# Performance work log

Hardware: AMD Instinct MI355X
Metric: run time of the kernel (lower is better)

## Reference

```python
import jax, jax.numpy as jnp
import numpy as np

N_ITER = 12
LR_PRIMAL = 0.5
LR_DUAL = 0.8
LAM_CLIP = 1e6
SLACK_EPS = 1e-8


def setup_inputs() -> dict:
    key = jax.random.key(0)
    k1, k2, k3 = jax.random.split(key, 3)
    B, n_gen = 65536, 256
    p_pred = jax.random.normal(k1, (B, n_gen), dtype=jnp.float32)
    p_min = jnp.zeros((n_gen,), dtype=jnp.float32)
    # generator upper limits in (1, 11)
    p_max = 1.0 + 10.0 * jax.random.uniform(k2, (n_gen,), dtype=jnp.float32)
    # total load roughly feasible: fraction of total capacity
    total_load = jax.random.uniform(k3, (B,), dtype=jnp.float32) * jnp.sum(p_max) * 0.5
    return {"p_pred": p_pred, "total_load": total_load, "p_min": p_min, "p_max": p_max}


def _dc_feasibility(p_pred, total_load, p_min, p_max):
    # p_pred: (B, n_gen); total_load: (B,)
    load = total_load[:, None]            # (B, 1)
    pmin = p_min[None, :]                 # (1, n_gen)
    pmax = p_max[None, :]
    p = p_pred
    lam = jnp.zeros((p.shape[0], 1), dtype=p.dtype)
    for _ in range(N_ITER):  # fixed unrolled primal-dual iterations
        grad = (p - p_pred) + lam
        p = p - LR_PRIMAL * grad
        p = jnp.clip(p, pmin, pmax)
        res = jnp.sum(p, axis=1, keepdims=True) - load
        lam = jnp.clip(lam + LR_DUAL * res, -LAM_CLIP, LAM_CLIP)
    # final slack redistribution among strictly-interior generators
    res = jnp.sum(p, axis=1, keepdims=True) - load
    slack_mask = ((p > pmin + SLACK_EPS) & (p < pmax - SLACK_EPS)).astype(p.dtype)
    slack_sum = jnp.sum(slack_mask, axis=1, keepdims=True)
    slack_sum = jnp.where(slack_sum == 0, jnp.ones_like(slack_sum), slack_sum)
    p = p - (res / slack_sum) * slack_mask
    return p


def reference(p_pred, total_load, p_min, p_max):
    return _dc_feasibility(p_pred, total_load, p_min, p_max)
```

## Files before the change

### kernel.cpp

```cpp
#include <hip/hip_runtime.h>

#define NITER 12

typedef float v2f __attribute__((ext_vector_type(2)));

__device__ __forceinline__ float dpp_ror_add(float x, const int ctrl_base) {
    int xi = __builtin_bit_cast(int, x);
    int yi;
    switch (ctrl_base) {
      case 8: yi = __builtin_amdgcn_update_dpp(0, xi, 0x128, 0xf, 0xf, true); break;
      case 4: yi = __builtin_amdgcn_update_dpp(0, xi, 0x124, 0xf, 0xf, true); break;
      case 2: yi = __builtin_amdgcn_update_dpp(0, xi, 0x122, 0xf, 0xf, true); break;
      default: yi = __builtin_amdgcn_update_dpp(0, xi, 0x121, 0xf, 0xf, true); break;
    }
    return x + __builtin_bit_cast(float, yi);
}

__global__ __launch_bounds__(256, 8) void dc_feas_kernel(
    const float* __restrict__ p_pred,
    const float* __restrict__ total_load,
    const float* __restrict__ p_min,
    const float* __restrict__ p_max,
    float* __restrict__ out, int B)
{
#pragma clang fp contract(off)
    const int lane = threadIdx.x & 63;
    const int wave = threadIdx.x >> 6;
    const int r    = lane >> 5;
    const int t    = lane & 31;

    const int row = (blockIdx.x << 3) + (wave << 1) + r;
    if (row >= B) return;

    const size_t base = (size_t)row * 256;
    const int e0 = t << 2;

    const float4 a0 = *(const float4*)(p_pred + base + e0);
    const float4 a1 = *(const float4*)(p_pred + base + e0 + 128);
    const float4 h0 = *(const float4*)(p_max + e0);
    const float4 h1 = *(const float4*)(p_max + e0 + 128);

    v2f PR[4], HI[4], P[4];
    PR[0] = (v2f){a0.x, a1.x}; PR[1] = (v2f){a0.y, a1.y};
    PR[2] = (v2f){a0.z, a1.z}; PR[3] = (v2f){a0.w, a1.w};
    HI[0] = (v2f){h0.x, h1.x}; HI[1] = (v2f){h0.y, h1.y};
    HI[2] = (v2f){h0.z, h1.z}; HI[3] = (v2f){h0.w, h1.w};

    const float load = total_load[row];

    auto rowsum = [&](const v2f* v) -> float {
        const v2f A = (v[0] + v[1]) + (v[2] + v[3]);
        float s = A.x + A.y;
        s += __shfl_xor(s, 16, 64);
        s = dpp_ror_add(s, 8);
        s = dpp_ror_add(s, 4);
        s = dpp_ror_add(s, 2);
        s = dpp_ror_add(s, 1);
        return s;
    };

#pragma unroll
    for (int j = 0; j < 4; ++j) {
        P[j].x = __builtin_amdgcn_fmed3f(PR[j].x, 0.0f, HI[j].x);
        P[j].y = __builtin_amdgcn_fmed3f(PR[j].y, 0.0f, HI[j].y);
    }
    float res = rowsum(P) - load;
    float lam = __builtin_amdgcn_fmed3f(0.8f * res, -1000000.0f, 1000000.0f);

    for (int it = 1; it < NITER; ++it) {
        const v2f lam2  = (v2f){lam, lam};
        const v2f mhalf = (v2f){-0.5f, -0.5f};
#pragma unroll
        for (int j = 0; j < 4; ++j) {
            const v2f g  = (P[j] - PR[j]) + lam2;
            const v2f pn = __builtin_elementwise_fma(g, mhalf, P[j]);
            P[j].x = __builtin_amdgcn_fmed3f(pn.x, 0.0f, HI[j].x);
            P[j].y = __builtin_amdgcn_fmed3f(pn.y, 0.0f, HI[j].y);
        }
        res = rowsum(P) - load;
        const float dl = 0.8f * res;
        lam = __builtin_amdgcn_fmed3f(lam + dl, -1000000.0f, 1000000.0f);
    }

    v2f M[4];
#pragma unroll
    for (int j = 0; j < 4; ++j) {
        M[j].x = (P[j].x > 1e-8f && P[j].x < HI[j].x - 1e-8f) ? 1.0f : 0.0f;
        M[j].y = (P[j].y > 1e-8f && P[j].y < HI[j].y - 1e-8f) ? 1.0f : 0.0f;
    }
    float ss = rowsum(M);
    ss = (ss == 0.0f) ? 1.0f : ss;
    const float adj = res / ss;

    const v2f madj2 = (v2f){-adj, -adj};
    v2f O[4];
#pragma unroll
    for (int j = 0; j < 4; ++j)
        O[j] = __builtin_elementwise_fma(M[j], madj2, P[j]);

    float4 o;
    o.x = O[0].x; o.y = O[1].x; o.z = O[2].x; o.w = O[3].x;
    *(float4*)(out + base + e0) = o;
    o.x = O[0].y; o.y = O[1].y; o.z = O[2].y; o.w = O[3].y;
    *(float4*)(out + base + e0 + 128) = o;
}

extern "C" void kernel_launch(void* const* d_in, const int* in_sizes, int n_in,
                              void* d_out, int out_size, void* d_ws, size_t ws_size,
                              hipStream_t stream) {
    const float* p_pred     = (const float*)d_in[0];
    const float* total_load = (const float*)d_in[1];
    const float* p_min      = (const float*)d_in[2];
    const float* p_max      = (const float*)d_in[3];
    float* out = (float*)d_out;

    const int B = in_sizes[1];
    const int rows_per_block = 8;
    const int grid = (B + rows_per_block - 1) / rows_per_block;

    dc_feas_kernel<<<grid, 256, 0, stream>>>(p_pred, total_load, p_min, p_max, out, B);
}
```

Before: 121.2 us.

## Use persistent grid-stride waves with software-prefetched next row pair

Replaces the one-row-pair-per-wave launch with a fixed grid of 2048 blocks in which each wave loops over row pairs with a grid stride. The next pair's p_pred and load values are loaded before the current pair is computed, so global-memory latency overlaps the iterative compute. The aim is to cut launch and tail overhead and hide memory stalls. In exchange it adds register pressure for the prefetch buffers and drops the bounds handling for odd B or waves with no work.

```diff
diff --git a/kernel.cpp b/kernel.cpp
--- a/kernel.cpp
+++ b/kernel.cpp
@@ -28,25 +28,17 @@
     const int wave = threadIdx.x >> 6;
     const int r    = lane >> 5;
     const int t    = lane & 31;
+    const int e0   = t << 2;
 
-    const int row = (blockIdx.x << 3) + (wave << 1) + r;
-    if (row >= B) return;
+    const int w     = (blockIdx.x << 2) + wave;
+    const int NW    = gridDim.x << 2;
+    const int npair = B >> 1;
 
-    const size_t base = (size_t)row * 256;
-    const int e0 = t << 2;
-
-    const float4 a0 = *(const float4*)(p_pred + base + e0);
-    const float4 a1 = *(const float4*)(p_pred + base + e0 + 128);
     const float4 h0 = *(const float4*)(p_max + e0);
     const float4 h1 = *(const float4*)(p_max + e0 + 128);
-
-    v2f PR[4], HI[4], P[4];
-    PR[0] = (v2f){a0.x, a1.x}; PR[1] = (v2f){a0.y, a1.y};
-    PR[2] = (v2f){a0.z, a1.z}; PR[3] = (v2f){a0.w, a1.w};
+    v2f HI[4];
     HI[0] = (v2f){h0.x, h1.x}; HI[1] = (v2f){h0.y, h1.y};
     HI[2] = (v2f){h0.z, h1.z}; HI[3] = (v2f){h0.w, h1.w};
-
-    const float load = total_load[row];
 
     auto rowsum = [&](const v2f* v) -> float {
         const v2f A = (v[0] + v[1]) + (v[2] + v[3]);
@@ -59,50 +51,81 @@
         return s;
     };
 
-#pragma unroll
-    for (int j = 0; j < 4; ++j) {
-        P[j].x = __builtin_amdgcn_fmed3f(PR[j].x, 0.0f, HI[j].x);
-        P[j].y = __builtin_amdgcn_fmed3f(PR[j].y, 0.0f, HI[j].y);
+    int bp = w;
+    float4 c0, c1; float cld;
+    {
+        const size_t cb = (size_t)(bp * 2 + r) * 256 + e0;
+        c0 = *(const float4*)(p_pred + cb);
+        c1 = *(const float4*)(p_pred + cb + 128);
+        cld = total_load[bp * 2 + r];
     }
-    float res = rowsum(P) - load;
-    float lam = __builtin_amdgcn_fmed3f(0.8f * res, -1000000.0f, 1000000.0f);
 
-    for (int it = 1; it < NITER; ++it) {
-        const v2f lam2  = (v2f){lam, lam};
-        const v2f mhalf = (v2f){-0.5f, -0.5f};
+    for (;;) {
+        const int nxt = bp + NW;
+        const bool has_nxt = nxt < npair;
+        float4 n0, n1; float nld;
+        if (has_nxt) {
+            const size_t nb = (size_t)(nxt * 2 + r) * 256 + e0;
+            n0 = *(const float4*)(p_pred + nb);
+            n1 = *(const float4*)(p_pred + nb + 128);
+            nld = total_load[nxt * 2 + r];
+        }
+
+        v2f PR[4], P[4];
+        PR[0] = (v2f){c0.x, c1.x}; PR[1] = (v2f){c0.y, c1.y};
+        PR[2] = (v2f){c0.z, c1.z}; PR[3] = (v2f){c0.w, c1.w};
+        const float load = cld;
+        const size_t base = (size_t)(bp * 2 + r) * 256;
+
 #pragma unroll
         for (int j = 0; j < 4; ++j) {
-            const v2f g  = (P[j] - PR[j]) + lam2;
-            const v2f pn = __builtin_elementwise_fma(g, mhalf, P[j]);
-            P[j].x = __builtin_amdgcn_fmed3f(pn.x, 0.0f, HI[j].x);
-            P[j].y = __builtin_amdgcn_fmed3f(pn.y, 0.0f, HI[j].y);
+            P[j].x = __builtin_amdgcn_fmed3f(PR[j].x, 0.0f, HI[j].x);
+            P[j].y = __builtin_amdgcn_fmed3f(PR[j].y, 0.0f, HI[j].y);
         }
-        res = rowsum(P) - load;
-        const float dl = 0.8f * res;
-        lam = __builtin_amdgcn_fmed3f(lam + dl, -1000000.0f, 1000000.0f);
+        float res = rowsum(P) - load;
+        float lam = __builtin_amdgcn_fmed3f(0.8f * res, -1000000.0f, 1000000.0f);
+
+        for (int it = 1; it < NITER; ++it) {
+            const v2f lam2  = (v2f){lam, lam};
+            const v2f mhalf = (v2f){-0.5f, -0.5f};
+#pragma unroll
+            for (int j = 0; j < 4; ++j) {
+                const v2f g  = (P[j] - PR[j]) + lam2;
+                const v2f pn = __builtin_elementwise_fma(g, mhalf, P[j]);
+                P[j].x = __builtin_amdgcn_fmed3f(pn.x, 0.0f, HI[j].x);
+                P[j].y = __builtin_amdgcn_fmed3f(pn.y, 0.0f, HI[j].y);
+            }
+            res = rowsum(P) - load;
+            const float dl = 0.8f * res;
+            lam = __builtin_amdgcn_fmed3f(lam + dl, -1000000.0f, 1000000.0f);
+        }
+
+        v2f M[4];
+#pragma unroll
+        for (int j = 0; j < 4; ++j) {
+            M[j].x = (P[j].x > 1e-8f && P[j].x < HI[j].x - 1e-8f) ? 1.0f : 0.0f;
+            M[j].y = (P[j].y > 1e-8f && P[j].y < HI[j].y - 1e-8f) ? 1.0f : 0.0f;
+        }
+        float ss = rowsum(M);
+        ss = (ss == 0.0f) ? 1.0f : ss;
+        const float adj = res / ss;
+
+        const v2f madj2 = (v2f){-adj, -adj};
+        v2f O[4];
+#pragma unroll
+        for (int j = 0; j < 4; ++j)
+            O[j] = __builtin_elementwise_fma(M[j], madj2, P[j]);
+
+        float4 o;
+        o.x = O[0].x; o.y = O[1].x; o.z = O[2].x; o.w = O[3].x;
+        *(float4*)(out + base + e0) = o;
+        o.x = O[0].y; o.y = O[1].y; o.z = O[2].y; o.w = O[3].y;
+        *(float4*)(out + base + e0 + 128) = o;
+
+        if (!has_nxt) break;
+        c0 = n0; c1 = n1; cld = nld;
+        bp = nxt;
     }
-
-    v2f M[4];
-#pragma unroll
-    for (int j = 0; j < 4; ++j) {
-        M[j].x = (P[j].x > 1e-8f && P[j].x < HI[j].x - 1e-8f) ? 1.0f : 0.0f;
-        M[j].y = (P[j].y > 1e-8f && P[j].y < HI[j].y - 1e-8f) ? 1.0f : 0.0f;
-    }
-    float ss = rowsum(M);
-    ss = (ss == 0.0f) ? 1.0f : ss;
-    const float adj = res / ss;
-
-    const v2f madj2 = (v2f){-adj, -adj};
-    v2f O[4];
-#pragma unroll
-    for (int j = 0; j < 4; ++j)
-        O[j] = __builtin_elementwise_fma(M[j], madj2, P[j]);
-
-    float4 o;
-    o.x = O[0].x; o.y = O[1].x; o.z = O[2].x; o.w = O[3].x;
-    *(float4*)(out + base + e0) = o;
-    o.x = O[0].y; o.y = O[1].y; o.z = O[2].y; o.w = O[3].y;
-    *(float4*)(out + base + e0 + 128) = o;
 }
 
 extern "C" void kernel_launch(void* const* d_in, const int* in_sizes, int n_in,
@@ -115,8 +138,5 @@
     float* out = (float*)d_out;
 
     const int B = in_sizes[1];
-    const int rows_per_block = 8;
-    const int grid = (B + rows_per_block - 1) / rows_per_block;
-
-    dc_feas_kernel<<<grid, 256, 0, stream>>>(p_pred, total_load, p_min, p_max, out, B);
+    dc_feas_kernel<<<2048, 256, 0, stream>>>(p_pred, total_load, p_min, p_max, out, B);
 }
```

Result: slower. 124.8 us (+3.0%).
